# Kernel tuning notes

Measured on AMD Instinct MI355X. Metric: run time of the kernel, lower is better.

Reference implementation:

```python
import jax, jax.numpy as jnp
import numpy as np

N, E, B, F_IN, C, K = 200000, 3200000, 128, 128, 10, 30
D_CAT = 97  # 32+32+32+1 concatenated GCN outputs


def setup_inputs() -> dict:
    key = jax.random.key(0)
    ks = jax.random.split(key, 12)
    s = 0.1
    return {
        "x": jax.random.normal(ks[0], (N, F_IN), jnp.float32),
        "edge_index": jax.random.randint(ks[1], (2, E), 0, N, jnp.int32),
        "batch": jnp.sort(jax.random.randint(ks[2], (N,), 0, B, jnp.int32)),
        "W1": jax.random.normal(ks[3], (F_IN, 32), jnp.float32) * s,
        "b1": jnp.zeros((32,), jnp.float32),
        "W2": jax.random.normal(ks[4], (32, 32), jnp.float32) * s,
        "b2": jnp.zeros((32,), jnp.float32),
        "W3": jax.random.normal(ks[5], (32, 32), jnp.float32) * s,
        "b3": jnp.zeros((32,), jnp.float32),
        "W4": jax.random.normal(ks[6], (32, 1), jnp.float32) * s,
        "b4": jnp.zeros((1,), jnp.float32),
        "conv5_w": jax.random.normal(ks[7], (16, 1, 97), jnp.float32) * s,
        "conv5_b": jnp.zeros((16,), jnp.float32),
        "conv6_w": jax.random.normal(ks[8], (32, 16, 5), jnp.float32) * s,
        "conv6_b": jnp.zeros((32,), jnp.float32),
        "fc1_w": jax.random.normal(ks[9], (352, 128), jnp.float32) * s,
        "fc1_b": jnp.zeros((128,), jnp.float32),
        "fc2_w": jax.random.normal(ks[10], (128, C), jnp.float32) * s,
        "fc2_b": jnp.zeros((C,), jnp.float32),
    }


def _gcn(x, W, b, src, dst, enorm, self_norm):
    # PyG GCNConv: h = xW; out = sum_j norm_ij * h_j (incl. self loop) + b
    h = x @ W
    agg = jax.ops.segment_sum(h[src] * enorm[:, None], dst, num_segments=h.shape[0])
    return agg + h * self_norm[:, None] + b


def _conv1d(x, w, b, stride):
    y = jax.lax.conv_general_dilated(x, w, (stride,), 'VALID',
                                     dimension_numbers=('NCH', 'OIH', 'NCH'))
    return y + b[None, :, None]


def reference(x, edge_index, batch, W1, b1, W2, b2, W3, b3, W4, b4,
              conv5_w, conv5_b, conv6_w, conv6_b, fc1_w, fc1_b, fc2_w, fc2_b):
    src, dst = edge_index[0], edge_index[1]
    # remove_self_loops (zero edge weight) then GCN adds self loop of weight 1
    w = (src != dst).astype(x.dtype)
    deg = jax.ops.segment_sum(w, dst, num_segments=N) + 1.0
    dinv = jax.lax.rsqrt(deg)
    enorm = w * dinv[src] * dinv[dst]   # per-edge sym norm
    self_norm = 1.0 / deg               # self-loop norm = dinv[i]^2

    x1 = jnp.tanh(_gcn(x, W1, b1, src, dst, enorm, self_norm))
    x2 = jnp.tanh(_gcn(x1, W2, b2, src, dst, enorm, self_norm))
    x3 = jnp.tanh(_gcn(x2, W3, b3, src, dst, enorm, self_norm))
    x4 = jnp.tanh(_gcn(x3, W4, b4, src, dst, enorm, self_norm))
    xc = jnp.concatenate([x1, x2, x3, x4], axis=-1)  # [N, 97]

    # SortAggregation(k=30): per-graph top-k nodes by last channel (descending)
    keyf = xc[:, -1]
    graph_ids = jnp.arange(B, dtype=batch.dtype)
    scores = jnp.where(batch[None, :] == graph_ids[:, None], keyf[None, :],
                       jnp.float32(-jnp.inf))         # [B, N]
    topv, topi = jax.lax.top_k(scores, K)              # [B, K]
    feats = xc[topi]                                   # [B, K, 97]
    feats = jnp.where(jnp.isfinite(topv)[..., None], feats, 0.0)  # pad rows -> 0
    z = feats.reshape(B, 1, K * D_CAT)                 # [B, 1, 2910]

    z = jax.nn.relu(_conv1d(z, conv5_w, conv5_b, 97))  # [B, 16, 30]
    z = jax.lax.reduce_window(z, -jnp.inf, jax.lax.max,
                              (1, 1, 2), (1, 1, 2), 'VALID')  # [B, 16, 15]
    z = jax.nn.relu(_conv1d(z, conv6_w, conv6_b, 1))   # [B, 32, 11]
    z = z.reshape(B, -1)                               # [B, 352]
    h = jax.nn.relu(z @ fc1_w + fc1_b)                 # dropout = identity (eval)
    return jax.nn.log_softmax(h @ fc2_w + fc2_b, axis=-1)
```

## Files before the change

### kernel.cpp

```cpp
#include <hip/hip_runtime.h>
#include <math.h>

#define TPB 256
#define TOPK 30
#define NGRAPH 128
#define TKCAP 4096
#define BSHIFT 11
#define NBMAX 128
#define FSHIFT 8
#define NFMAX 800
#define FCAP 4608


__global__ void bhist(const int* __restrict__ src, const int* __restrict__ dst,
                      int* __restrict__ btot, int E) {
    __shared__ int bcnt[NBMAX];
    int t = threadIdx.x;
    int base = blockIdx.x * 2048;
    int lim = E - base; if (lim > 2048) lim = 2048;
    for (int i = t; i < NBMAX; i += 256) bcnt[i] = 0;
    __syncthreads();
    for (int i = t; i < lim; i += 256) {
        int s = src[base + i], d = dst[base + i];
        if (s != d) atomicAdd(&bcnt[d >> BSHIFT], 1);
    }
    __syncthreads();
    for (int i = t; i < NBMAX; i += 256)
        if (bcnt[i] > 0) atomicAdd(&btot[i], bcnt[i]);
}

__global__ void bucket_scan(const int* __restrict__ btot, int* __restrict__ bbase,
                            int nbuckets) {
    __shared__ int ls[NBMAX];
    int t = threadIdx.x;
    int v = (t < nbuckets) ? btot[t] : 0;
    ls[t] = v;
    __syncthreads();
    for (int o = 1; o < NBMAX; o <<= 1) {
        int x = 0;
        if (t >= o) x = ls[t - o];
        __syncthreads();
        ls[t] += x;
        __syncthreads();
    }
    if (t < nbuckets) bbase[t] = ls[t] - v;
}

__global__ void bin_edges(const int* __restrict__ src, const int* __restrict__ dst,
                          const int* __restrict__ bbase_g, int* __restrict__ gcur,
                          int2* __restrict__ scratch, int E) {
    __shared__ int2 eds[2048];
    __shared__ int bcnt[NBMAX], bbase[NBMAX], boff[NBMAX];
    int t = threadIdx.x;
    int base = blockIdx.x * 2048;
    int lim = E - base; if (lim > 2048) lim = 2048;
    for (int i = t; i < NBMAX; i += 256) { bcnt[i] = 0; boff[i] = 0; }
    __syncthreads();
    for (int i = t; i < lim; i += 256) {
        int s = src[base + i], d = dst[base + i];
        if (s == d) d = -1;
        eds[i] = make_int2(s, d);
        if (d >= 0) atomicAdd(&bcnt[d >> BSHIFT], 1);
    }
    __syncthreads();
    for (int i = t; i < NBMAX; i += 256) {
        if (bcnt[i] > 0)
            bbase[i] = bbase_g[i] + atomicAdd(&gcur[i], bcnt[i]);
    }
    __syncthreads();
    for (int i = t; i < lim; i += 256) {
        int2 ed = eds[i];
        if (ed.y >= 0) {
            int b = ed.y >> BSHIFT;
            int pos = bbase[b] + atomicAdd(&boff[b], 1);
            scratch[pos] = ed;
        }
    }
}

__global__ void bucket_count(const int2* __restrict__ scratch,
                             const int* __restrict__ bbase, const int* __restrict__ btot,
                             int* __restrict__ rowptr, float* __restrict__ dinv,
                             float* __restrict__ snorm, int N, int NB) {
    __shared__ int hist[1 << BSHIFT];
    __shared__ int ls2[256];
    int b = blockIdx.x, t = threadIdx.x;
    int nlo = b << BSHIFT;
    int nn = N - nlo; if (nn > (1 << BSHIFT)) nn = 1 << BSHIFT;
    for (int i = t; i < (1 << BSHIFT); i += 256) hist[i] = 0;
    __syncthreads();
    int lo = bbase[b], hi = lo + btot[b];
    for (int e = lo + t; e < hi; e += 256)
        atomicAdd(&hist[scratch[e].y - nlo], 1);
    __syncthreads();
    int loc[8]; int run = 0;
    #pragma unroll
    for (int j = 0; j < 8; ++j) { loc[j] = run; run += hist[t * 8 + j]; }
    ls2[t] = run;
    __syncthreads();
    for (int o = 1; o < 256; o <<= 1) {
        int x = (t >= o) ? ls2[t - o] : 0;
        __syncthreads();
        ls2[t] += x;
        __syncthreads();
    }
    int base = bbase[b] + ls2[t] - run;
    #pragma unroll
    for (int j = 0; j < 8; ++j) {
        int i = t * 8 + j;
        if (i < nn) {
            rowptr[nlo + i] = base + loc[j];
            int c = hist[i];
            float deg = (float)c + 1.0f;
            dinv[nlo + i] = 1.0f / sqrtf(deg);
            snorm[nlo + i] = 1.0f / deg;
        }
    }
    if (b == NB - 1 && t == 0) rowptr[N] = bbase[b] + btot[b];
}

__global__ void bin2(const int2* __restrict__ scratch, const int* __restrict__ rowptr,
                     int* __restrict__ fcur, int2* __restrict__ scratch2, int N, int E) {
    __shared__ int fcnt[NFMAX], fbase[NFMAX], foff[NFMAX];
    int t = threadIdx.x;
    int En = rowptr[N];
    int base = blockIdx.x * 8192;
    if (base >= En) return;
    int lim = En - base; if (lim > 8192) lim = 8192;
    for (int i = t; i < NFMAX; i += 256) { fcnt[i] = 0; foff[i] = 0; }
    __syncthreads();
    for (int i = t; i < lim; i += 256) {
        int d = scratch[base + i].y;
        atomicAdd(&fcnt[d >> FSHIFT], 1);
    }
    __syncthreads();
    for (int fi = t; fi < NFMAX; fi += 256) {
        if (fcnt[fi] > 0)
            fbase[fi] = rowptr[fi << FSHIFT] + atomicAdd(&fcur[fi], fcnt[fi]);
    }
    __syncthreads();
    for (int i = t; i < lim; i += 256) {
        int2 ed = scratch[base + i];
        int fi = ed.y >> FSHIFT;
        int pos = fbase[fi] + atomicAdd(&foff[fi], 1);
        scratch2[pos] = ed;
    }
}

__global__ __launch_bounds__(256) void scatter_sort(const int2* __restrict__ scratch2,
                                                    const int* __restrict__ rowptr,
                                                    const float* __restrict__ dinv,
                                                    int2* __restrict__ eprec, int N) {
    __shared__ int srcA[FCAP], dstA[FCAP], inv[FCAP];
    __shared__ int hist[1 << FSHIFT];
    __shared__ int hcur[1 << FSHIFT];
    int f = blockIdx.x, t = threadIdx.x;
    int nlo = f << FSHIFT;
    int nhi = nlo + (1 << FSHIFT); if (nhi > N) nhi = N;
    int lo = rowptr[nlo], hi = rowptr[nhi];
    int span = hi - lo;
    for (int i = t; i < (1 << FSHIFT); i += 256) hist[i] = 0;
    __syncthreads();
    if (span <= FCAP) {
        for (int i = t; i < span; i += 256) {
            int2 ed = scratch2[lo + i];
            srcA[i] = ed.x; dstA[i] = ed.y;
            atomicAdd(&hist[ed.y - nlo], 1);
        }
        __syncthreads();
        int v = hist[t];
        hcur[t] = v;
        __syncthreads();
        for (int o = 1; o < 256; o <<= 1) {
            int x = (t >= o) ? hcur[t - o] : 0;
            __syncthreads();
            hcur[t] += x;
            __syncthreads();
        }
        int excl = hcur[t] - v;
        __syncthreads();
        hcur[t] = excl;
        __syncthreads();
        for (int i = t; i < span; i += 256) {
            int slot = atomicAdd(&hcur[dstA[i] - nlo], 1);
            inv[slot] = i;
        }
        __syncthreads();
        for (int p = t; p < span; p += 256) {
            int i = inv[p];
            int s = srcA[i], d = dstA[i];
            eprec[lo + p] = make_int2(s, __float_as_int(dinv[s] * dinv[d]));
        }
    } else {
        for (int e = lo + t; e < hi; e += 256) {
            int2 ed = scratch2[e];
            int d = ed.y;
            int p = rowptr[d] + atomicAdd(&hist[d - nlo], 1);
            eprec[p] = make_int2(ed.x, __float_as_int(dinv[ed.x] * dinv[d]));
        }
    }
}


__global__ void mm_128_32(const float* __restrict__ X, const float* __restrict__ W,
                          float* __restrict__ H, int n) {
    __shared__ float Ws[128 * 32];
    __shared__ float xs[32 * 128];
    int t = threadIdx.x;
    int rbase = blockIdx.x * 32;
    #pragma unroll
    for (int j = 0; j < 4; ++j) {
        int idx = t + 256 * j;
        *(float4*)(Ws + idx * 4) = *(const float4*)(W + idx * 4);
        int row = rbase + (idx >> 5);
        float4 v = make_float4(0.f, 0.f, 0.f, 0.f);
        if (row < n) v = *(const float4*)(X + (long)rbase * 128 + idx * 4);
        *(float4*)(xs + idx * 4) = v;
    }
    __syncthreads();
    int c4 = (t & 7) * 4, r = t >> 3;
    int row = rbase + r;
    if (row >= n) return;
    float ac0 = 0.f, ac1 = 0.f, ac2 = 0.f, ac3 = 0.f;
    #pragma unroll 8
    for (int k0 = 0; k0 < 128; k0 += 4) {
        float4 xv = *(const float4*)(xs + r * 128 + k0);
        #pragma unroll
        for (int j = 0; j < 4; ++j) {
            float xj = (j == 0) ? xv.x : (j == 1) ? xv.y : (j == 2) ? xv.z : xv.w;
            float4 wv = *(const float4*)(Ws + (k0 + j) * 32 + c4);
            ac0 += xj * wv.x; ac1 += xj * wv.y; ac2 += xj * wv.z; ac3 += xj * wv.w;
        }
    }
    *(float4*)(H + (long)row * 32 + c4) = make_float4(ac0, ac1, ac2, ac3);
}

__global__ void mm_32_32(const float* __restrict__ X, const float* __restrict__ W,
                         float* __restrict__ H, int n) {
    __shared__ float Ws[32 * 32];
    __shared__ float xs[32 * 32];
    int t = threadIdx.x;
    int rbase = blockIdx.x * 32;
    {
        *(float4*)(Ws + t * 4) = *(const float4*)(W + t * 4);
        int row = rbase + (t >> 3);
        float4 v = make_float4(0.f, 0.f, 0.f, 0.f);
        if (row < n) v = *(const float4*)(X + (long)rbase * 32 + t * 4);
        *(float4*)(xs + t * 4) = v;
    }
    __syncthreads();
    int c4 = (t & 7) * 4, r = t >> 3;
    int row = rbase + r;
    if (row >= n) return;
    float ac0 = 0.f, ac1 = 0.f, ac2 = 0.f, ac3 = 0.f;
    #pragma unroll
    for (int k0 = 0; k0 < 32; k0 += 4) {
        float4 xv = *(const float4*)(xs + r * 32 + k0);
        #pragma unroll
        for (int j = 0; j < 4; ++j) {
            float xj = (j == 0) ? xv.x : (j == 1) ? xv.y : (j == 2) ? xv.z : xv.w;
            float4 wv = *(const float4*)(Ws + (k0 + j) * 32 + c4);
            ac0 += xj * wv.x; ac1 += xj * wv.y; ac2 += xj * wv.z; ac3 += xj * wv.w;
        }
    }
    *(float4*)(H + (long)row * 32 + c4) = make_float4(ac0, ac1, ac2, ac3);
}

__global__ void mm_32_1(const float* __restrict__ X, const float* __restrict__ W,
                        float* __restrict__ H4, int n) {
    int gid = blockIdx.x * blockDim.x + threadIdx.x;
    int node = gid >> 3, l = gid & 7;
    if (node >= n) return;
    float4 v = *(const float4*)(X + (long)node * 32 + l * 4);
    float s = v.x * W[l * 4] + v.y * W[l * 4 + 1] + v.z * W[l * 4 + 2] + v.w * W[l * 4 + 3];
    s += __shfl_xor(s, 1, 64);
    s += __shfl_xor(s, 2, 64);
    s += __shfl_xor(s, 4, 64);
    if (l == 0) H4[node] = s;
}


__global__ void agg32(const float* __restrict__ H, const int2* __restrict__ eprec,
                      const int* __restrict__ rowptr,
                      const float* __restrict__ snorm, const float* __restrict__ bias,
                      float* __restrict__ OUT, int n) {
    int gid = blockIdx.x * blockDim.x + threadIdx.x;
    int node = gid >> 3, l = gid & 7;
    if (node >= n) return;
    int beg = rowptr[node], end = rowptr[node + 1];
    float ax = 0.f, ay = 0.f, az = 0.f, aw = 0.f;
    int e0 = beg;
    for (; e0 + 8 <= end; e0 += 8) {
        int2 ed = eprec[e0 + l];
        int ss[8]; float ww[8];
        #pragma unroll
        for (int j = 0; j < 8; ++j) {
            ss[j] = __shfl(ed.x, j, 8);
            ww[j] = __shfl(__int_as_float(ed.y), j, 8);
        }
        float4 hv[8];
        #pragma unroll
        for (int j = 0; j < 8; ++j)
            hv[j] = *(const float4*)(H + (long)ss[j] * 32 + l * 4);
        #pragma unroll
        for (int j = 0; j < 8; ++j) {
            ax += hv[j].x * ww[j]; ay += hv[j].y * ww[j];
            az += hv[j].z * ww[j]; aw += hv[j].w * ww[j];
        }
    }
    if (e0 < end) {
        int m = end - e0;
        int2 ed = (l < m) ? eprec[e0 + l] : make_int2(0, 0);
        for (int j = 0; j < m; ++j) {
            int s = __shfl(ed.x, j, 8);
            float w = __shfl(__int_as_float(ed.y), j, 8);
            float4 hv = *(const float4*)(H + (long)s * 32 + l * 4);
            ax += hv.x * w; ay += hv.y * w; az += hv.z * w; aw += hv.w * w;
        }
    }
    float sn = snorm[node];
    float4 hv = *(const float4*)(H + (long)node * 32 + l * 4);
    float4 bv = *(const float4*)(bias + l * 4);
    float4 o;
    o.x = tanhf(ax + hv.x * sn + bv.x);
    o.y = tanhf(ay + hv.y * sn + bv.y);
    o.z = tanhf(az + hv.z * sn + bv.z);
    o.w = tanhf(aw + hv.w * sn + bv.w);
    *(float4*)(OUT + (long)node * 32 + l * 4) = o;
}

__global__ void agg1(const float* __restrict__ H4, const int2* __restrict__ eprec,
                     const int* __restrict__ rowptr,
                     const float* __restrict__ snorm, const float* __restrict__ b4,
                     float* __restrict__ X4, int n) {
    int node = blockIdx.x * blockDim.x + threadIdx.x;
    if (node >= n) return;
    int beg = rowptr[node], end = rowptr[node + 1];
    float acc = 0.f;
    for (int e = beg; e < end; ++e) {
        int2 ed = eprec[e];
        acc += H4[ed.x] * __int_as_float(ed.y);
    }
    X4[node] = tanhf(acc + H4[node] * snorm[node] + b4[0]);
}


__global__ void graph_start(const int* __restrict__ batch, int* __restrict__ gstart,
                            int n, int B) {
    int i = blockIdx.x * blockDim.x + threadIdx.x;
    if (i >= n) return;
    int b = batch[i];
    int bp = (i == 0) ? -1 : batch[i - 1];
    for (int g = bp + 1; g <= b; ++g) gstart[g] = i;
    if (i == n - 1) {
        for (int g = b + 1; g <= B; ++g) gstart[g] = n;
    }
}


#define GTP(av,ai,bv,bi) (((av) > (bv)) || ((av) == (bv) && (ai) < (bi)))

__device__ __forceinline__ void bsort256(float& v0, float& v1, float& v2, float& v3,
                                         int& i0, int& i1, int& i2, int& i3, int lane) {
    for (int k = 2; k <= 256; k <<= 1) {
        for (int j = k >> 1; j > 0; j >>= 1) {
            if (j == 64) {
                { bool down = ((lane) & k) == 0;
                  bool agt = GTP(v0, i0, v1, i1);
                  if (down != agt) { float tv = v0; v0 = v1; v1 = tv; int ti = i0; i0 = i1; i1 = ti; } }
                { bool down = ((lane + 128) & k) == 0;
                  bool agt = GTP(v2, i2, v3, i3);
                  if (down != agt) { float tv = v2; v2 = v3; v3 = tv; int ti = i2; i2 = i3; i3 = ti; } }
            } else if (j == 128) {
                { bool down = ((lane) & k) == 0;
                  bool agt = GTP(v0, i0, v2, i2);
                  if (down != agt) { float tv = v0; v0 = v2; v2 = tv; int ti = i0; i0 = i2; i2 = ti; } }
                { bool down = ((lane + 64) & k) == 0;
                  bool agt = GTP(v1, i1, v3, i3);
                  if (down != agt) { float tv = v1; v1 = v3; v3 = tv; int ti = i1; i1 = i3; i3 = ti; } }
            } else {
                #define XSTEP(vv, ii, ebase) { \
                    float ov = __shfl_xor(vv, j, 64); \
                    int   oi = __shfl_xor(ii, j, 64); \
                    bool down = ((lane + (ebase)) & k) == 0; \
                    bool low  = (lane & j) == 0; \
                    bool win  = GTP(vv, ii, ov, oi); \
                    bool keep = (down == low) ? win : !win; \
                    if (!keep) { vv = ov; ii = oi; } }
                XSTEP(v0, i0, 0) XSTEP(v1, i1, 64) XSTEP(v2, i2, 128) XSTEP(v3, i3, 192)
                #undef XSTEP
            }
        }
    }
}


__global__ __launch_bounds__(512) void topk_head(
        const float* __restrict__ x1, const float* __restrict__ x2,
        const float* __restrict__ x3, const float* __restrict__ x4,
        const int* __restrict__ gstart,
        const float* __restrict__ w5, const float* __restrict__ b5,
        const float* __restrict__ w6, const float* __restrict__ b6,
        const float* __restrict__ fw1, const float* __restrict__ fb1,
        const float* __restrict__ fw2, const float* __restrict__ fb2,
        float* __restrict__ out) {
    int g = blockIdx.x;
    int t = threadIdx.x;
    __shared__ int topi_l[TOPK];
    __shared__ int selg[TOPK];
    __shared__ float lv[8 * TOPK];
    __shared__ int li[8 * TOPK];
    __shared__ float vals[TKCAP];
    __shared__ float wbv[8];
    __shared__ int wbi[8];
    __shared__ float ws5[16 * 97];
    __shared__ float ws6[32 * 16 * 5];
    __shared__ float wf2[128 * 10];
    __shared__ float part[4][128];
    __shared__ float feats[TOPK][97];
    __shared__ float c5[16][30];
    __shared__ float p6[16][15];
    __shared__ float z[352];
    __shared__ float hh[128];
    __shared__ float oo[10];

    int beg = gstart[g], end = gstart[g + 1];
    int range = end - beg;

    if (range <= 2048) {
        int wv = t >> 6, lane = t & 63;
        int csz = (range + 7) >> 3;
        int cbeg = wv * csz;
        float v0, v1, v2, v3; int j0, j1, j2, j3;
        {
            int id0 = lane, id1 = lane + 64, id2 = lane + 128, id3 = lane + 192;
            bool k0 = (id0 < csz) && (cbeg + id0 < range);
            bool k1 = (id1 < csz) && (cbeg + id1 < range);
            bool k2 = (id2 < csz) && (cbeg + id2 < range);
            bool k3 = (id3 < csz) && (cbeg + id3 < range);
            v0 = k0 ? x4[beg + cbeg + id0] : -INFINITY;
            v1 = k1 ? x4[beg + cbeg + id1] : -INFINITY;
            v2 = k2 ? x4[beg + cbeg + id2] : -INFINITY;
            v3 = k3 ? x4[beg + cbeg + id3] : -INFINITY;
            j0 = k0 ? (cbeg + id0) : (0x0FFFF000 + id0);
            j1 = k1 ? (cbeg + id1) : (0x0FFFF000 + id1);
            j2 = k2 ? (cbeg + id2) : (0x0FFFF000 + id2);
            j3 = k3 ? (cbeg + id3) : (0x0FFFF000 + id3);
        }
        bsort256(v0, v1, v2, v3, j0, j1, j2, j3, lane);
        if (lane < TOPK) { lv[wv * TOPK + lane] = v0; li[wv * TOPK + lane] = j0; }
        __syncthreads();
        if (t < 64) {
            float m0, m1, m2, m3; int n0, n1, n2, n3;
            int id0 = t, id1 = t + 64, id2 = t + 128, id3 = t + 192;
            m0 = (id0 < 8 * TOPK) ? lv[id0] : -INFINITY;
            m1 = (id1 < 8 * TOPK) ? lv[id1] : -INFINITY;
            m2 = (id2 < 8 * TOPK) ? lv[id2] : -INFINITY;
            m3 = (id3 < 8 * TOPK) ? lv[id3] : -INFINITY;
            n0 = (id0 < 8 * TOPK) ? li[id0] : (0x0FFFF000 + id0);
            n1 = (id1 < 8 * TOPK) ? li[id1] : (0x0FFFF000 + id1);
            n2 = (id2 < 8 * TOPK) ? li[id2] : (0x0FFFF000 + id2);
            n3 = (id3 < 8 * TOPK) ? li[id3] : (0x0FFFF000 + id3);
            bsort256(m0, m1, m2, m3, n0, n1, n2, n3, t);
            if (t < TOPK)
                topi_l[t] = (m0 == -INFINITY) ? -1 : beg + n0;
        } else {
            int u = t - 64;
            for (int i = u; i < 16 * 97; i += 448) ws5[i] = w5[i];
            for (int i = u; i < 32 * 16 * 5; i += 448) ws6[i] = w6[i];
            for (int i = u; i < 128 * 10; i += 448) wf2[i] = fw2[i];
        }
    } else {
        if (t >= 256) {
            int u = t - 256;
            for (int i = u; i < 16 * 97; i += 256) ws5[i] = w5[i];
            for (int i = u; i < 32 * 16 * 5; i += 256) ws6[i] = w6[i];
            for (int i = u; i < 128 * 10; i += 256) wf2[i] = fw2[i];
        }
        int lim = range < TKCAP ? range : TKCAP;
        for (int i = t; i < lim; i += 512) vals[i] = x4[beg + i];
        __syncthreads();
        for (int k = 0; k < TOPK; ++k) {
            float best = -INFINITY;
            int bi = 0x7fffffff;
            for (int i = t; i < lim; i += 512) {
                float v = vals[i];
                if (v > best) { best = v; bi = i; }
            }
            for (int i = TKCAP + t; i < range; i += 512) {
                int gi = beg + i;
                bool taken = false;
                for (int j = 0; j < k; ++j)
                    if (selg[j] == gi) { taken = true; break; }
                if (taken) continue;
                float v = x4[gi];
                if (v > best || (v == best && i < bi)) { best = v; bi = i; }
            }
            #pragma unroll
            for (int off = 1; off < 64; off <<= 1) {
                float ov = __shfl_xor(best, off, 64);
                int oi = __shfl_xor(bi, off, 64);
                if (ov > best || (ov == best && oi < bi)) { best = ov; bi = oi; }
            }
            if ((t & 63) == 0) { wbv[t >> 6] = best; wbi[t >> 6] = bi; }
            __syncthreads();
            if (t == 0) {
                float bv = wbv[0]; int bi0 = wbi[0];
                for (int wq = 1; wq < 8; ++wq)
                    if (wbv[wq] > bv || (wbv[wq] == bv && wbi[wq] < bi0)) { bv = wbv[wq]; bi0 = wbi[wq]; }
                int gl = (bi0 == 0x7fffffff) ? -1 : beg + bi0;
                selg[k] = gl;
                topi_l[k] = gl;
                if (bi0 != 0x7fffffff && bi0 < TKCAP) vals[bi0] = -INFINITY;
            }
            __syncthreads();
        }
    }
    __syncthreads();

    for (int idx = t; idx < TOPK * 97; idx += 512) {
        int k = idx / 97, j = idx % 97;
        int node = topi_l[k];
        float v = 0.f;
        if (node >= 0) {
            if (j < 32) v = x1[(long)node * 32 + j];
            else if (j < 64) v = x2[(long)node * 32 + (j - 32)];
            else if (j < 96) v = x3[(long)node * 32 + (j - 64)];
            else v = x4[node];
        }
        feats[k][j] = v;
    }
    __syncthreads();

    for (int idx = t; idx < 16 * 30; idx += 512) {
        int oc = idx / 30, k = idx % 30;
        float acc = b5[oc];
        for (int j = 0; j < 97; ++j) acc += ws5[oc * 97 + j] * feats[k][j];
        c5[oc][k] = fmaxf(acc, 0.f);
    }
    __syncthreads();

    for (int idx = t; idx < 16 * 15; idx += 512) {
        int oc = idx / 15, k = idx % 15;
        p6[oc][k] = fmaxf(c5[oc][2 * k], c5[oc][2 * k + 1]);
    }
    __syncthreads();

    for (int idx = t; idx < 32 * 11; idx += 512) {
        int oc = idx / 11, tt = idx % 11;
        float acc = b6[oc];
        for (int ic = 0; ic < 16; ++ic)
            for (int j = 0; j < 5; ++j)
                acc += ws6[(oc * 16 + ic) * 5 + j] * p6[ic][tt + j];
        z[idx] = fmaxf(acc, 0.f);
    }
    __syncthreads();

    {
        int o = t & 127, s = t >> 7;
        float acc = 0.f;
        int i0 = s * 88, i1 = i0 + 88;
        for (int i = i0; i < i1; ++i) acc += z[i] * fw1[i * 128 + o];
        part[s][o] = acc;
    }
    __syncthreads();
    if (t < 128) {
        float v = fb1[t] + ((part[0][t] + part[1][t]) + (part[2][t] + part[3][t]));
        hh[t] = fmaxf(v, 0.f);
    }
    __syncthreads();

    if (t < 10) {
        float acc = fb2[t];
        for (int j = 0; j < 128; ++j) acc += hh[j] * wf2[j * 10 + t];
        oo[t] = acc;
    }
    __syncthreads();

    if (t < 10) {
        float m = -INFINITY;
        for (int c = 0; c < 10; ++c) m = fmaxf(m, oo[c]);
        float s = 0.f;
        for (int c = 0; c < 10; ++c) s += expf(oo[c] - m);
        out[g * 10 + t] = oo[t] - m - logf(s);
    }
}


extern "C" void kernel_launch(void* const* d_in, const int* in_sizes, int n_in,
                              void* d_out, int out_size, void* d_ws, size_t ws_size,
                              hipStream_t stream) {
    const float* x     = (const float*)d_in[0];
    const int*   ei    = (const int*)d_in[1];
    const int*   batch = (const int*)d_in[2];
    const float* W1 = (const float*)d_in[3];
    const float* b1 = (const float*)d_in[4];
    const float* W2 = (const float*)d_in[5];
    const float* b2 = (const float*)d_in[6];
    const float* W3 = (const float*)d_in[7];
    const float* b3 = (const float*)d_in[8];
    const float* W4 = (const float*)d_in[9];
    const float* b4 = (const float*)d_in[10];
    const float* w5 = (const float*)d_in[11];
    const float* b5 = (const float*)d_in[12];
    const float* w6 = (const float*)d_in[13];
    const float* b6 = (const float*)d_in[14];
    const float* fw1 = (const float*)d_in[15];
    const float* fb1 = (const float*)d_in[16];
    const float* fw2 = (const float*)d_in[17];
    const float* fb2 = (const float*)d_in[18];

    const int N = in_sizes[0] / 128;
    const int E = in_sizes[1] / 2;
    const int* src = ei;
    const int* dst = ei + E;

    char* w = (char*)d_ws;
    size_t off = 0;
    auto alloc = [&](size_t bytes) -> void* {
        void* p = w + off;
        off = (off + bytes + 255) & ~(size_t)255;
        return p;
    };

    int*   gcur   = (int*)alloc(NBMAX * 4);
    int*   btot   = (int*)alloc(NBMAX * 4);
    int*   fcur   = (int*)alloc(NFMAX * 4);
    int*   bbase  = (int*)alloc(NBMAX * 4);
    int*   gstart = (int*)alloc((size_t)(NGRAPH + 1) * 4);
    int*   rowptr = (int*)alloc((size_t)(N + 1) * 4);
    float* dinv   = (float*)alloc((size_t)N * 4);
    float* snorm  = (float*)alloc((size_t)N * 4);
    int2*  eprec  = (int2*)alloc((size_t)E * 8);
    float* hbuf   = (float*)alloc((size_t)N * 32 * 4);
    float* x1     = (float*)alloc((size_t)N * 32 * 4);
    float* x2     = (float*)alloc((size_t)N * 32 * 4);
    float* x3     = (float*)alloc((size_t)N * 32 * 4);
    float* h4     = (float*)alloc((size_t)N * 4);
    float* x4     = (float*)alloc((size_t)N * 4);

    int2* scratch  = (int2*)hbuf;
    int2* scratch2 = (int2*)x1;

    hipMemsetAsync(gcur, 0, (size_t)(2 * NBMAX + NFMAX) * 4, stream);

    const int NB = (N + (1 << BSHIFT) - 1) >> BSHIFT;
    const int NF = (N + (1 << FSHIFT) - 1) >> FSHIFT;
    const int EB = (E + 2047) / 2048;

    graph_start<<<(N + TPB - 1) / TPB, TPB, 0, stream>>>(batch, gstart, N, NGRAPH);
    bhist<<<EB, TPB, 0, stream>>>(src, dst, btot, E);
    bucket_scan<<<1, NBMAX, 0, stream>>>(btot, bbase, NB);
    bin_edges<<<EB, TPB, 0, stream>>>(src, dst, bbase, gcur, scratch, E);
    bucket_count<<<NB, TPB, 0, stream>>>(scratch, bbase, btot, rowptr, dinv, snorm, N, NB);
    bin2<<<(E + 8191) / 8192, TPB, 0, stream>>>(scratch, rowptr, fcur, scratch2, N, E);
    scatter_sort<<<NF, 256, 0, stream>>>(scratch2, rowptr, dinv, eprec, N);

    mm_128_32<<<(N + 31) / 32, 256, 0, stream>>>(x, W1, hbuf, N);
    agg32<<<((size_t)N * 8 + TPB - 1) / TPB, TPB, 0, stream>>>(hbuf, eprec, rowptr,
                                                               snorm, b1, x1, N);
    mm_32_32<<<(N + 31) / 32, 256, 0, stream>>>(x1, W2, hbuf, N);
    agg32<<<((size_t)N * 8 + TPB - 1) / TPB, TPB, 0, stream>>>(hbuf, eprec, rowptr,
                                                               snorm, b2, x2, N);
    mm_32_32<<<(N + 31) / 32, 256, 0, stream>>>(x2, W3, hbuf, N);
    agg32<<<((size_t)N * 8 + TPB - 1) / TPB, TPB, 0, stream>>>(hbuf, eprec, rowptr,
                                                               snorm, b3, x3, N);
    mm_32_1<<<((size_t)N * 8 + TPB - 1) / TPB, TPB, 0, stream>>>(x3, W4, h4, N);
    agg1<<<(N + TPB - 1) / TPB, TPB, 0, stream>>>(h4, eprec, rowptr, snorm, b4, x4, N);

    topk_head<<<NGRAPH, 512, 0, stream>>>(x1, x2, x3, x4, gstart,
                                          w5, b5, w6, b6, fw1, fb1, fw2, fb2,
                                          (float*)d_out);
}
```

Before: 549.1 us.

## Pack edge records into single ints, fuse graph_start into bhist, unroll aggregation

Binned edge records are packed into one 32-bit int (src shifted with low destination bits), halving scratch traffic through bin_edges, bucket_count, bin2 and scatter_sort. bin2 recovers the coarse bucket with a binary search over bucket bases, since the high destination bits are dropped. The graph_start kernel is merged into the bhist launch as extra blocks to save a launch. The agg32 inner loop gains a 16-edge unrolled stage that issues more independent gathers per iteration. The packing assumes src fits in 21 bits and raises register pressure in the aggregation.

```diff
diff --git a/kernel.cpp b/kernel.cpp
--- a/kernel.cpp
+++ b/kernel.cpp
@@ -12,11 +12,25 @@
 #define FCAP 4608
 
 
-__global__ void bhist(const int* __restrict__ src, const int* __restrict__ dst,
-                      int* __restrict__ btot, int E) {
+__global__ void bhist_gs(const int* __restrict__ src, const int* __restrict__ dst,
+                         int* __restrict__ btot, int E, int EB,
+                         const int* __restrict__ batch, int* __restrict__ gstart,
+                         int n, int B) {
+    int blk = blockIdx.x;
+    if (blk >= EB) {
+        int i = (blk - EB) * blockDim.x + threadIdx.x;
+        if (i >= n) return;
+        int b = batch[i];
+        int bp = (i == 0) ? -1 : batch[i - 1];
+        for (int g = bp + 1; g <= b; ++g) gstart[g] = i;
+        if (i == n - 1) {
+            for (int g = b + 1; g <= B; ++g) gstart[g] = n;
+        }
+        return;
+    }
     __shared__ int bcnt[NBMAX];
     int t = threadIdx.x;
-    int base = blockIdx.x * 2048;
+    int base = blk * 2048;
     int lim = E - base; if (lim > 2048) lim = 2048;
     for (int i = t; i < NBMAX; i += 256) bcnt[i] = 0;
     __syncthreads();
@@ -48,8 +62,9 @@
 
 __global__ void bin_edges(const int* __restrict__ src, const int* __restrict__ dst,
                           const int* __restrict__ bbase_g, int* __restrict__ gcur,
-                          int2* __restrict__ scratch, int E) {
-    __shared__ int2 eds[2048];
+                          int* __restrict__ scratch, int E) {
+    __shared__ int eds[2048];
+    __shared__ unsigned char ebk[2048];
     __shared__ int bcnt[NBMAX], bbase[NBMAX], boff[NBMAX];
     int t = threadIdx.x;
     int base = blockIdx.x * 2048;
@@ -58,9 +73,13 @@
     __syncthreads();
     for (int i = t; i < lim; i += 256) {
         int s = src[base + i], d = dst[base + i];
-        if (s == d) d = -1;
-        eds[i] = make_int2(s, d);
-        if (d >= 0) atomicAdd(&bcnt[d >> BSHIFT], 1);
+        if (s == d) { ebk[i] = 255; }
+        else {
+            int b = d >> BSHIFT;
+            ebk[i] = (unsigned char)b;
+            eds[i] = (s << BSHIFT) | (d & ((1 << BSHIFT) - 1));
+            atomicAdd(&bcnt[b], 1);
+        }
     }
     __syncthreads();
     for (int i = t; i < NBMAX; i += 256) {
@@ -69,16 +88,15 @@
     }
     __syncthreads();
     for (int i = t; i < lim; i += 256) {
-        int2 ed = eds[i];
-        if (ed.y >= 0) {
-            int b = ed.y >> BSHIFT;
+        if (ebk[i] != 255) {
+            int b = ebk[i];
             int pos = bbase[b] + atomicAdd(&boff[b], 1);
-            scratch[pos] = ed;
-        }
-    }
-}
-
-__global__ void bucket_count(const int2* __restrict__ scratch,
+            scratch[pos] = eds[i];
+        }
+    }
+}
+
+__global__ void bucket_count(const int* __restrict__ scratch,
                              const int* __restrict__ bbase, const int* __restrict__ btot,
                              int* __restrict__ rowptr, float* __restrict__ dinv,
                              float* __restrict__ snorm, int N, int NB) {
@@ -91,7 +109,7 @@
     __syncthreads();
     int lo = bbase[b], hi = lo + btot[b];
     for (int e = lo + t; e < hi; e += 256)
-        atomicAdd(&hist[scratch[e].y - nlo], 1);
+        atomicAdd(&hist[scratch[e] & ((1 << BSHIFT) - 1)], 1);
     __syncthreads();
     int loc[8]; int run = 0;
     #pragma unroll
@@ -119,19 +137,28 @@
     if (b == NB - 1 && t == 0) rowptr[N] = bbase[b] + btot[b];
 }
 
-__global__ void bin2(const int2* __restrict__ scratch, const int* __restrict__ rowptr,
-                     int* __restrict__ fcur, int2* __restrict__ scratch2, int N, int E) {
+__global__ void bin2(const int* __restrict__ scratch, const int* __restrict__ bbase_g,
+                     const int* __restrict__ rowptr,
+                     int* __restrict__ fcur, int* __restrict__ scratch2, int N, int NB) {
     __shared__ int fcnt[NFMAX], fbase[NFMAX], foff[NFMAX];
+    __shared__ int bb[NBMAX];
+    __shared__ unsigned short fid[8192];
     int t = threadIdx.x;
     int En = rowptr[N];
     int base = blockIdx.x * 8192;
     if (base >= En) return;
     int lim = En - base; if (lim > 8192) lim = 8192;
+    for (int i = t; i < NBMAX; i += 256) bb[i] = (i < NB) ? bbase_g[i] : 0x7fffffff;
     for (int i = t; i < NFMAX; i += 256) { fcnt[i] = 0; foff[i] = 0; }
     __syncthreads();
     for (int i = t; i < lim; i += 256) {
-        int d = scratch[base + i].y;
-        atomicAdd(&fcnt[d >> FSHIFT], 1);
+        int gi = base + i;
+        int lo = 0, hi = NB - 1;
+        while (lo < hi) { int m = (lo + hi + 1) >> 1; if (bb[m] <= gi) lo = m; else hi = m - 1; }
+        int e = scratch[gi];
+        int fi = (lo << (BSHIFT - FSHIFT)) | ((e >> FSHIFT) & ((1 << (BSHIFT - FSHIFT)) - 1));
+        fid[i] = (unsigned short)fi;
+        atomicAdd(&fcnt[fi], 1);
     }
     __syncthreads();
     for (int fi = t; fi < NFMAX; fi += 256) {
@@ -140,18 +167,19 @@
     }
     __syncthreads();
     for (int i = t; i < lim; i += 256) {
-        int2 ed = scratch[base + i];
-        int fi = ed.y >> FSHIFT;
+        int e = scratch[base + i];
+        int fi = fid[i];
+        int pf = ((e >> BSHIFT) << FSHIFT) | (e & ((1 << FSHIFT) - 1));
         int pos = fbase[fi] + atomicAdd(&foff[fi], 1);
-        scratch2[pos] = ed;
-    }
-}
-
-__global__ __launch_bounds__(256) void scatter_sort(const int2* __restrict__ scratch2,
+        scratch2[pos] = pf;
+    }
+}
+
+__global__ __launch_bounds__(256) void scatter_sort(const int* __restrict__ scratch2,
                                                     const int* __restrict__ rowptr,
                                                     const float* __restrict__ dinv,
                                                     int2* __restrict__ eprec, int N) {
-    __shared__ int srcA[FCAP], dstA[FCAP], inv[FCAP];
+    __shared__ int pA[FCAP], inv[FCAP];
     __shared__ int hist[1 << FSHIFT];
     __shared__ int hcur[1 << FSHIFT];
     int f = blockIdx.x, t = threadIdx.x;
@@ -159,13 +187,13 @@
     int nhi = nlo + (1 << FSHIFT); if (nhi > N) nhi = N;
     int lo = rowptr[nlo], hi = rowptr[nhi];
     int span = hi - lo;
-    for (int i = t; i < (1 << FSHIFT); i += 256) hist[i] = 0;
+    hist[t] = 0;
     __syncthreads();
     if (span <= FCAP) {
         for (int i = t; i < span; i += 256) {
-            int2 ed = scratch2[lo + i];
-            srcA[i] = ed.x; dstA[i] = ed.y;
-            atomicAdd(&hist[ed.y - nlo], 1);
+            int e = scratch2[lo + i];
+            pA[i] = e;
+            atomicAdd(&hist[e & 255], 1);
         }
         __syncthreads();
         int v = hist[t];
@@ -182,21 +210,21 @@
         hcur[t] = excl;
         __syncthreads();
         for (int i = t; i < span; i += 256) {
-            int slot = atomicAdd(&hcur[dstA[i] - nlo], 1);
+            int slot = atomicAdd(&hcur[pA[i] & 255], 1);
             inv[slot] = i;
         }
         __syncthreads();
         for (int p = t; p < span; p += 256) {
-            int i = inv[p];
-            int s = srcA[i], d = dstA[i];
+            int e = pA[inv[p]];
+            int s = e >> FSHIFT, d = nlo | (e & 255);
             eprec[lo + p] = make_int2(s, __float_as_int(dinv[s] * dinv[d]));
         }
     } else {
-        for (int e = lo + t; e < hi; e += 256) {
-            int2 ed = scratch2[e];
-            int d = ed.y;
-            int p = rowptr[d] + atomicAdd(&hist[d - nlo], 1);
-            eprec[p] = make_int2(ed.x, __float_as_int(dinv[ed.x] * dinv[d]));
+        for (int e0 = lo + t; e0 < hi; e0 += 256) {
+            int e = scratch2[e0];
+            int s = e >> FSHIFT, d = nlo | (e & 255);
+            int p = rowptr[d] + atomicAdd(&hist[e & 255], 1);
+            eprec[p] = make_int2(s, __float_as_int(dinv[s] * dinv[d]));
         }
     }
 }
@@ -290,6 +318,27 @@
     int beg = rowptr[node], end = rowptr[node + 1];
     float ax = 0.f, ay = 0.f, az = 0.f, aw = 0.f;
     int e0 = beg;
+    for (; e0 + 16 <= end; e0 += 16) {
+        int2 ed0 = eprec[e0 + l];
+        int2 ed1 = eprec[e0 + 8 + l];
+        int ss[16]; float ww[16];
+        #pragma unroll
+        for (int j = 0; j < 8; ++j) {
+            ss[j] = __shfl(ed0.x, j, 8);
+            ww[j] = __shfl(__int_as_float(ed0.y), j, 8);
+            ss[8 + j] = __shfl(ed1.x, j, 8);
+            ww[8 + j] = __shfl(__int_as_float(ed1.y), j, 8);
+        }
+        float4 hv[16];
+        #pragma unroll
+        for (int j = 0; j < 16; ++j)
+            hv[j] = *(const float4*)(H + (long)ss[j] * 32 + l * 4);
+        #pragma unroll
+        for (int j = 0; j < 16; ++j) {
+            ax += hv[j].x * ww[j]; ay += hv[j].y * ww[j];
+            az += hv[j].z * ww[j]; aw += hv[j].w * ww[j];
+        }
+    }
     for (; e0 + 8 <= end; e0 += 8) {
         int2 ed = eprec[e0 + l];
         int ss[8]; float ww[8];
@@ -342,19 +391,6 @@
         acc += H4[ed.x] * __int_as_float(ed.y);
     }
     X4[node] = tanhf(acc + H4[node] * snorm[node] + b4[0]);
-}
-
-
-__global__ void graph_start(const int* __restrict__ batch, int* __restrict__ gstart,
-                            int n, int B) {
-    int i = blockIdx.x * blockDim.x + threadIdx.x;
-    if (i >= n) return;
-    int b = batch[i];
-    int bp = (i == 0) ? -1 : batch[i - 1];
-    for (int g = bp + 1; g <= b; ++g) gstart[g] = i;
-    if (i == n - 1) {
-        for (int g = b + 1; g <= B; ++g) gstart[g] = n;
-    }
 }
 
 
@@ -639,21 +675,21 @@
     float* h4     = (float*)alloc((size_t)N * 4);
     float* x4     = (float*)alloc((size_t)N * 4);
 
-    int2* scratch  = (int2*)hbuf;
-    int2* scratch2 = (int2*)x1;
+    int* scratch  = (int*)hbuf;
+    int* scratch2 = (int*)x1;
 
     hipMemsetAsync(gcur, 0, (size_t)(2 * NBMAX + NFMAX) * 4, stream);
 
     const int NB = (N + (1 << BSHIFT) - 1) >> BSHIFT;
     const int NF = (N + (1 << FSHIFT) - 1) >> FSHIFT;
     const int EB = (E + 2047) / 2048;
-
-    graph_start<<<(N + TPB - 1) / TPB, TPB, 0, stream>>>(batch, gstart, N, NGRAPH);
-    bhist<<<EB, TPB, 0, stream>>>(src, dst, btot, E);
+    const int GB = (N + TPB - 1) / TPB;
+
+    bhist_gs<<<EB + GB, TPB, 0, stream>>>(src, dst, btot, E, EB, batch, gstart, N, NGRAPH);
     bucket_scan<<<1, NBMAX, 0, stream>>>(btot, bbase, NB);
     bin_edges<<<EB, TPB, 0, stream>>>(src, dst, bbase, gcur, scratch, E);
     bucket_count<<<NB, TPB, 0, stream>>>(scratch, bbase, btot, rowptr, dinv, snorm, N, NB);
-    bin2<<<(E + 8191) / 8192, TPB, 0, stream>>>(scratch, rowptr, fcur, scratch2, N, E);
+    bin2<<<(E + 8191) / 8192, TPB, 0, stream>>>(scratch, bbase, rowptr, fcur, scratch2, N, NB);
     scatter_sort<<<NF, 256, 0, stream>>>(scratch2, rowptr, dinv, eprec, N);
 
     mm_128_32<<<(N + 31) / 32, 256, 0, stream>>>(x, W1, hbuf, N);
```

New measurement: 551.1 us. No clear change (+0.4%).
